# Performance work log

Measured on AMD Instinct MI355X. Metric: run time of the kernel, lower is better.

The kernel has to match this reference:

```python
import jax, jax.numpy as jnp
import numpy as np

EPS = 1e-12  # F.normalize eps

def _l2norm(x, axis=-1):
    n = jnp.linalg.norm(x, axis=axis, keepdims=True)
    return x / jnp.maximum(n, EPS)

def setup_inputs() -> dict:
    key = jax.random.key(0)
    k1, k2 = jax.random.split(key)
    Q, D = 512, 1024
    B, L = 64, 1024
    queries = jax.random.normal(k1, (Q, D), dtype=jnp.float32)
    local_tokens = jax.random.normal(k2, (B, L, D), dtype=jnp.float32)
    return {"queries": queries, "local_tokens": local_tokens}

def reference(queries, local_tokens):
    # sim_op == 'dot', repeat == True, need_attn_weights == False
    D = local_tokens.shape[-1]
    denom = jnp.sqrt(jnp.asarray(D, dtype=queries.dtype))
    # scores: [B, Q, L] == bmm(expand(queries), local_tokens^T) / sqrt(D)
    scores = jnp.einsum('qd,bld->bql', queries, local_tokens) / denom
    attn = jax.nn.softmax(scores, axis=-1)
    # aggregated: [B, Q, D]
    agg = jnp.einsum('bql,bld->bqd', attn, local_tokens)
    # post L2-normalize both sides (query normalize is batch-invariant)
    qn = _l2norm(queries)          # [Q, D]
    aggn = _l2norm(agg)            # [B, Q, D]
    # per-(b,q) dot product -> [B, Q], then transpose -> [Q, B]
    logits = jnp.einsum('qd,bqd->bq', qn, aggn).T
    return logits
```

## Files before the change

### kernel.cpp

```cpp
#include <hip/hip_runtime.h>
#include <stdint.h>

#define QN 512
#define DN 1024
#define BN 64
#define LN 1024

typedef _Float16 f16x8 __attribute__((ext_vector_type(8)));
typedef _Float16 f16x4 __attribute__((ext_vector_type(4)));
typedef float f32x4 __attribute__((ext_vector_type(4)));

#define DMA16(gp, lp)                                                        \
  __builtin_amdgcn_global_load_lds(                                          \
      (const __attribute__((address_space(1))) uint32_t*)(const void*)(gp),  \
      (__attribute__((address_space(3))) uint32_t*)(void*)(lp), 16, 0, 0)

__global__ __launch_bounds__(256) void k_convert(const float* __restrict__ tok,
                                                 _Float16* __restrict__ T,
                                                 _Float16* __restrict__ TT) {
  __shared__ __align__(16) _Float16 tile[64][68];
  const int b = blockIdx.z;
  const int l0 = blockIdx.y * 64, d0 = blockIdx.x * 64;
  const int tid = threadIdx.x;
  const int rr = tid >> 4;
  const int cq = tid & 15;
  const size_t base = (size_t)b * LN * DN;
#pragma unroll
  for (int p = 0; p < 4; ++p) {
    const int l = p * 16 + rr;
    const float4 v = *(const float4*)(tok + base + (size_t)(l0 + l) * DN + d0 + cq * 4);
    f16x4 hv;
    hv[0] = (_Float16)v.x; hv[1] = (_Float16)v.y; hv[2] = (_Float16)v.z; hv[3] = (_Float16)v.w;
    *(f16x4*)(T + base + (size_t)(l0 + l) * DN + d0 + cq * 4) = hv;
    tile[cq * 4 + 0][l] = hv[0];
    tile[cq * 4 + 1][l] = hv[1];
    tile[cq * 4 + 2][l] = hv[2];
    tile[cq * 4 + 3][l] = hv[3];
  }
  __syncthreads();
  const size_t baseT = (size_t)b * DN * LN;
#pragma unroll
  for (int p = 0; p < 4; ++p) {
    const int d = p * 16 + rr;
    const f16x4 hv = *(const f16x4*)(&tile[d][cq * 4]);
    *(f16x4*)(TT + baseT + (size_t)(d0 + d) * LN + l0 + cq * 4) = hv;
  }
}

__global__ __launch_bounds__(256) void k_queries(const float* __restrict__ q,
                                                 _Float16* __restrict__ Qh,
                                                 float* __restrict__ invqn) {
  const int qr = blockIdx.x;
  const int tid = threadIdx.x;
  const float4 v = *(const float4*)(q + (size_t)qr * DN + tid * 4);
  float ss = v.x * v.x + v.y * v.y + v.z * v.z + v.w * v.w;
#pragma unroll
  for (int off = 1; off < 64; off <<= 1) ss += __shfl_xor(ss, off, 64);
  __shared__ float red[4];
  if ((tid & 63) == 0) red[tid >> 6] = ss;
  __syncthreads();
  const float tot = red[0] + red[1] + red[2] + red[3];
  f16x4 hv;
  hv[0] = (_Float16)v.x; hv[1] = (_Float16)v.y; hv[2] = (_Float16)v.z; hv[3] = (_Float16)v.w;
  *(f16x4*)(Qh + (size_t)qr * DN + tid * 4) = hv;
  if (tid == 0) invqn[qr] = 1.0f / fmaxf(sqrtf(tot), 1e-12f);
}

__device__ __forceinline__ void decode_bq(int g, int& b, int& q0) {
  const int xcd = g & 7;
  const int t = g >> 3;
  const int qt8 = t & 7;
  b = ((t >> 3) << 3) | xcd;
  q0 = qt8 * 64;
}

__global__ __launch_bounds__(512, 2) void k_scores(const _Float16* __restrict__ Qh,
                                                   const _Float16* __restrict__ T,
                                                   _Float16* __restrict__ P,
                                                   float* __restrict__ numv) {
  __shared__ __align__(16) _Float16 Bb[2][32768];
  __shared__ float maxbuf[8][64];
  __shared__ float sumbuf[8][64];
  __shared__ float numbuf[8][64];
  __shared__ float Mbuf[64];
  __shared__ float Rbuf[64];
  int b, q0;
  decode_bq(blockIdx.x, b, q0);
  const int tid = threadIdx.x;
  const int w = tid >> 6, lane = tid & 63, c = lane & 15, quad = lane >> 4;

  const char* __restrict__ gT = (const char*)(T + (size_t)b * LN * DN);
  const _Float16* __restrict__ gA = Qh + (size_t)q0 * DN;

  const int r4 = lane >> 2;
  const int qsw = ((lane & 3) - ((lane >> 3) & 3)) & 3;
  const char* gBbase = gT + (size_t)(w * 128 + r4) * 2048 + qsw * 16;

  const int bswz = ((quad + ((c >> 1) & 3)) & 3) * 8;
  const int boff = (w * 128 + c) * 32 + bswz;

  f32x4 acc[4][8];
#pragma unroll
  for (int i = 0; i < 4; ++i)
#pragma unroll
    for (int j = 0; j < 8; ++j) acc[i][j] = 0.f;

  const _Float16* gAl = gA + (size_t)c * DN + quad * 8;

  f16x8 a_cur[4], a_nxt[4];
#pragma unroll
  for (int qt = 0; qt < 4; ++qt) a_cur[qt] = *(const f16x8*)(gAl + (size_t)qt * 16 * DN);
#pragma unroll
  for (int j = 0; j < 8; ++j) DMA16(gBbase + (size_t)j * 32768, &Bb[0][(w * 8 + j) * 512]);

  for (int s = 0; s < 31; ++s) {
    const int cur = s & 1;
    const int sn = s + 1;
#pragma unroll
    for (int qt = 0; qt < 4; ++qt)
      a_nxt[qt] = *(const f16x8*)(gAl + (size_t)qt * 16 * DN + sn * 32);
    asm volatile("s_waitcnt lgkmcnt(0)" ::: "memory");
#pragma unroll
    for (int j = 0; j < 8; ++j)
      DMA16(gBbase + (size_t)j * 32768 + sn * 64, &Bb[cur ^ 1][(w * 8 + j) * 512]);
    asm volatile("s_waitcnt vmcnt(12)" ::: "memory");
    __builtin_amdgcn_sched_barrier(0);

    const _Float16* __restrict__ Bp = &Bb[cur][0];
#pragma unroll
    for (int lt = 0; lt < 8; ++lt) {
      const f16x8 bv = *(const f16x8*)(Bp + boff + lt * 512);
#pragma unroll
      for (int qt = 0; qt < 4; ++qt)
        acc[qt][lt] = __builtin_amdgcn_mfma_f32_16x16x32_f16(a_cur[qt], bv, acc[qt][lt], 0, 0, 0);
    }
#pragma unroll
    for (int qt = 0; qt < 4; ++qt) a_cur[qt] = a_nxt[qt];
  }
  asm volatile("s_waitcnt vmcnt(0)" ::: "memory");
  __builtin_amdgcn_sched_barrier(0);
  {
    const _Float16* __restrict__ Bp = &Bb[1][0];
#pragma unroll
    for (int lt = 0; lt < 8; ++lt) {
      const f16x8 bv = *(const f16x8*)(Bp + boff + lt * 512);
#pragma unroll
      for (int qt = 0; qt < 4; ++qt)
        acc[qt][lt] = __builtin_amdgcn_mfma_f32_16x16x32_f16(a_cur[qt], bv, acc[qt][lt], 0, 0, 0);
    }
  }

  float mx[4][4];
#pragma unroll
  for (int qt = 0; qt < 4; ++qt)
#pragma unroll
    for (int r = 0; r < 4; ++r) {
      float m = acc[qt][0][r];
#pragma unroll
      for (int lt = 1; lt < 8; ++lt) m = fmaxf(m, acc[qt][lt][r]);
      mx[qt][r] = m;
    }
#pragma unroll
  for (int off = 1; off < 16; off <<= 1)
#pragma unroll
    for (int qt = 0; qt < 4; ++qt)
#pragma unroll
      for (int r = 0; r < 4; ++r) mx[qt][r] = fmaxf(mx[qt][r], __shfl_xor(mx[qt][r], off, 64));
  if (c == 0)
#pragma unroll
    for (int qt = 0; qt < 4; ++qt)
#pragma unroll
      for (int r = 0; r < 4; ++r) maxbuf[w][qt * 16 + quad * 4 + r] = mx[qt][r];
  __syncthreads();
  if (tid < 64) {
    float m = maxbuf[0][tid];
#pragma unroll
    for (int ww = 1; ww < 8; ++ww) m = fmaxf(m, maxbuf[ww][tid]);
    Mbuf[tid] = m;
  }
  __syncthreads();

  const float KE = 0.045084220027780106f;
  float Mr[4][4], sl[4][4], nl[4][4];
#pragma unroll
  for (int qt = 0; qt < 4; ++qt)
#pragma unroll
    for (int r = 0; r < 4; ++r) {
      Mr[qt][r] = Mbuf[qt * 16 + quad * 4 + r];
      sl[qt][r] = 0.f;
      nl[qt][r] = 0.f;
    }
#pragma unroll
  for (int qt = 0; qt < 4; ++qt)
#pragma unroll
    for (int lt = 0; lt < 8; ++lt)
#pragma unroll
      for (int r = 0; r < 4; ++r) {
        const float u = acc[qt][lt][r];
        const float p = exp2f((u - Mr[qt][r]) * KE);
        acc[qt][lt][r] = p;
        sl[qt][r] += p;
        nl[qt][r] += p * u;
      }
#pragma unroll
  for (int off = 1; off < 16; off <<= 1)
#pragma unroll
    for (int qt = 0; qt < 4; ++qt)
#pragma unroll
      for (int r = 0; r < 4; ++r) {
        sl[qt][r] += __shfl_xor(sl[qt][r], off, 64);
        nl[qt][r] += __shfl_xor(nl[qt][r], off, 64);
      }
  if (c == 0)
#pragma unroll
    for (int qt = 0; qt < 4; ++qt)
#pragma unroll
      for (int r = 0; r < 4; ++r) {
        sumbuf[w][qt * 16 + quad * 4 + r] = sl[qt][r];
        numbuf[w][qt * 16 + quad * 4 + r] = nl[qt][r];
      }
  __syncthreads();
  if (tid < 64) {
    float S = 0.f, N = 0.f;
#pragma unroll
    for (int ww = 0; ww < 8; ++ww) {
      S += sumbuf[ww][tid];
      N += numbuf[ww][tid];
    }
    Rbuf[tid] = 1.0f / S;
    numv[(size_t)b * QN + q0 + tid] = N / S;
  }
  __syncthreads();

  _Float16* Pb = P + ((size_t)b * QN + q0) * LN;
#pragma unroll
  for (int qt = 0; qt < 4; ++qt)
#pragma unroll
    for (int r = 0; r < 4; ++r) {
      const int row = qt * 16 + quad * 4 + r;
      const float rS = Rbuf[row];
      _Float16* prow = Pb + (size_t)row * LN + c;
#pragma unroll
      for (int lt = 0; lt < 8; ++lt) prow[w * 128 + lt * 16] = (_Float16)(acc[qt][lt][r] * rS);
    }
}

__global__ __launch_bounds__(512, 2) void k_agg(const _Float16* __restrict__ P,
                                                const _Float16* __restrict__ TT,
                                                float* __restrict__ norm2) {
  __shared__ __align__(16) _Float16 Bb[2][32768];
  __shared__ float redbuf[8][64];
  int b, q0;
  decode_bq(blockIdx.x, b, q0);
  const int tid = threadIdx.x;
  const int w = tid >> 6, lane = tid & 63, c = lane & 15, quad = lane >> 4;

  const char* __restrict__ gT = (const char*)(TT + (size_t)b * DN * LN);
  const _Float16* __restrict__ gA = P + ((size_t)b * QN + q0) * LN;

  const int r4 = lane >> 2;
  const int qsw = ((lane & 3) - ((lane >> 3) & 3)) & 3;
  const char* gBbase = gT + (size_t)(w * 128 + r4) * 2048 + qsw * 16;

  const int bswz = ((quad + ((c >> 1) & 3)) & 3) * 8;
  const int boff = (w * 128 + c) * 32 + bswz;

  f32x4 acc[4][8];
#pragma unroll
  for (int i = 0; i < 4; ++i)
#pragma unroll
    for (int j = 0; j < 8; ++j) acc[i][j] = 0.f;

  const _Float16* gAl = gA + (size_t)c * LN + quad * 8;

  f16x8 a_cur[4], a_nxt[4];
#pragma unroll
  for (int qt = 0; qt < 4; ++qt) a_cur[qt] = *(const f16x8*)(gAl + (size_t)qt * 16 * LN);
#pragma unroll
  for (int j = 0; j < 8; ++j) DMA16(gBbase + (size_t)j * 32768, &Bb[0][(w * 8 + j) * 512]);

  for (int s = 0; s < 31; ++s) {
    const int cur = s & 1;
    const int sn = s + 1;
#pragma unroll
    for (int qt = 0; qt < 4; ++qt)
      a_nxt[qt] = *(const f16x8*)(gAl + (size_t)qt * 16 * LN + sn * 32);
    asm volatile("s_waitcnt lgkmcnt(0)" ::: "memory");
#pragma unroll
    for (int j = 0; j < 8; ++j)
      DMA16(gBbase + (size_t)j * 32768 + sn * 64, &Bb[cur ^ 1][(w * 8 + j) * 512]);
    asm volatile("s_waitcnt vmcnt(12)" ::: "memory");
    __builtin_amdgcn_sched_barrier(0);

    const _Float16* __restrict__ Bp = &Bb[cur][0];
#pragma unroll
    for (int dt = 0; dt < 8; ++dt) {
      const f16x8 bv = *(const f16x8*)(Bp + boff + dt * 512);
#pragma unroll
      for (int qt = 0; qt < 4; ++qt)
        acc[qt][dt] = __builtin_amdgcn_mfma_f32_16x16x32_f16(a_cur[qt], bv, acc[qt][dt], 0, 0, 0);
    }
#pragma unroll
    for (int qt = 0; qt < 4; ++qt) a_cur[qt] = a_nxt[qt];
  }
  asm volatile("s_waitcnt vmcnt(0)" ::: "memory");
  __builtin_amdgcn_sched_barrier(0);
  {
    const _Float16* __restrict__ Bp = &Bb[1][0];
#pragma unroll
    for (int dt = 0; dt < 8; ++dt) {
      const f16x8 bv = *(const f16x8*)(Bp + boff + dt * 512);
#pragma unroll
      for (int qt = 0; qt < 4; ++qt)
        acc[qt][dt] = __builtin_amdgcn_mfma_f32_16x16x32_f16(a_cur[qt], bv, acc[qt][dt], 0, 0, 0);
    }
  }

  float ss[4][4];
#pragma unroll
  for (int qt = 0; qt < 4; ++qt)
#pragma unroll
    for (int r = 0; r < 4; ++r) {
      float s = 0.f;
#pragma unroll
      for (int dt = 0; dt < 8; ++dt) {
        const float v = acc[qt][dt][r];
        s += v * v;
      }
      ss[qt][r] = s;
    }
#pragma unroll
  for (int off = 1; off < 16; off <<= 1)
#pragma unroll
    for (int qt = 0; qt < 4; ++qt)
#pragma unroll
      for (int r = 0; r < 4; ++r) ss[qt][r] += __shfl_xor(ss[qt][r], off, 64);
  if (c == 0)
#pragma unroll
    for (int qt = 0; qt < 4; ++qt)
#pragma unroll
      for (int r = 0; r < 4; ++r) redbuf[w][qt * 16 + quad * 4 + r] = ss[qt][r];
  __syncthreads();
  if (tid < 64) {
    float s = 0.f;
#pragma unroll
    for (int ww = 0; ww < 8; ++ww) s += redbuf[ww][tid];
    norm2[(size_t)b * QN + q0 + tid] = s;
  }
}

__global__ __launch_bounds__(256) void k_final(const float* __restrict__ numv,
                                               const float* __restrict__ norm2,
                                               const float* __restrict__ invqn,
                                               float* __restrict__ out) {
  const int idx = blockIdx.x * 256 + threadIdx.x;
  const int q = idx >> 6, b = idx & 63;
  const float n = numv[(size_t)b * QN + q];
  const float d = sqrtf(norm2[(size_t)b * QN + q]);
  out[idx] = n * invqn[q] / fmaxf(d, 1e-12f);
}

extern "C" void kernel_launch(void* const* d_in, const int* in_sizes, int n_in,
                              void* d_out, int out_size, void* d_ws, size_t ws_size,
                              hipStream_t stream) {
  (void)in_sizes; (void)n_in; (void)out_size; (void)ws_size;
  const float* queries = (const float*)d_in[0];
  const float* tok = (const float*)d_in[1];
  float* out = (float*)d_out;
  char* ws = (char*)d_ws;

  _Float16* TT = (_Float16*)(ws + 0);
  _Float16* T = (_Float16*)(ws + 134217728);
  _Float16* P = (_Float16*)(ws + 268435456);
  _Float16* Qh = (_Float16*)(ws + 335544320);
  float* invqn = (float*)(ws + 336592896);
  float* numv = (float*)(ws + 336594944);
  float* norm2 = (float*)(ws + 336726016);

  hipLaunchKernelGGL(k_convert, dim3(16, 16, 64), dim3(256), 0, stream, tok, T, TT);
  hipLaunchKernelGGL(k_queries, dim3(512), dim3(256), 0, stream, queries, Qh, invqn);
  hipLaunchKernelGGL(k_scores, dim3(512), dim3(512), 0, stream, Qh, T, P, numv);
  hipLaunchKernelGGL(k_agg, dim3(512), dim3(512), 0, stream, P, TT, norm2);
  hipLaunchKernelGGL(k_final, dim3(128), dim3(256), 0, stream, numv, norm2, invqn, out);
}
```

Baseline: 680.7 us.

## Replace LDS double buffer with three-slot half-tile ring in scores and agg GEMMs

Both GEMM kernels now split each K-step's B tile into two half-tiles streamed through a three-slot LDS ring (48 KB instead of 64 KB), issuing the next DMA into a slot right after its fragments are read into registers. The MFMA blocks are wrapped in workgroup barriers with raised wave priority to keep the waves of a block in step. This aims to deepen prefetch and cut LDS footprint so that global-load latency is better hidden behind MFMA work. The extra s_barrier pairs per half-step add synchronisation cost, and the hand-tuned vmcnt counts have to match the DMA ordering exactly.

Result: slower. 711.2 us (+4.5%).

```diff
diff --git a/kernel.cpp b/kernel.cpp
--- a/kernel.cpp
+++ b/kernel.cpp
@@ -14,6 +14,19 @@
   __builtin_amdgcn_global_load_lds(                                          \
       (const __attribute__((address_space(1))) uint32_t*)(const void*)(gp),  \
       (__attribute__((address_space(3))) uint32_t*)(void*)(lp), 16, 0, 0)
+
+#define SBAR() __builtin_amdgcn_s_barrier()
+#define SCHED0() __builtin_amdgcn_sched_barrier(0)
+#define WAIT_VM(n)                                             \
+  do {                                                         \
+    asm volatile("s_waitcnt vmcnt(" #n ")" ::: "memory");      \
+    __builtin_amdgcn_sched_barrier(0);                         \
+  } while (0)
+#define WAIT_LGKM0()                                           \
+  do {                                                         \
+    asm volatile("s_waitcnt lgkmcnt(0)" ::: "memory");         \
+    __builtin_amdgcn_sched_barrier(0);                         \
+  } while (0)
 
 __global__ __launch_bounds__(256) void k_convert(const float* __restrict__ tok,
                                                  _Float16* __restrict__ T,
@@ -78,7 +91,7 @@
                                                    const _Float16* __restrict__ T,
                                                    _Float16* __restrict__ P,
                                                    float* __restrict__ numv) {
-  __shared__ __align__(16) _Float16 Bb[2][32768];
+  __shared__ __align__(16) _Float16 ring[3][16384];
   __shared__ float maxbuf[8][64];
   __shared__ float sumbuf[8][64];
   __shared__ float numbuf[8][64];
@@ -97,7 +110,8 @@
   const char* gBbase = gT + (size_t)(w * 128 + r4) * 2048 + qsw * 16;
 
   const int bswz = ((quad + ((c >> 1) & 3)) & 3) * 8;
-  const int boff = (w * 128 + c) * 32 + bswz;
+  const int fragoff = c * 32 + bswz;
+  const int slab0 = w * 4;
 
   f32x4 acc[4][8];
 #pragma unroll
@@ -109,45 +123,101 @@
 
   f16x8 a_cur[4], a_nxt[4];
 #pragma unroll
+  for (int jj = 0; jj < 4; ++jj)
+    DMA16(gBbase + (size_t)jj * 32768, &ring[0][(slab0 + jj) * 512]);
+  SCHED0();
+#pragma unroll
   for (int qt = 0; qt < 4; ++qt) a_cur[qt] = *(const f16x8*)(gAl + (size_t)qt * 16 * DN);
-#pragma unroll
-  for (int j = 0; j < 8; ++j) DMA16(gBbase + (size_t)j * 32768, &Bb[0][(w * 8 + j) * 512]);
-
+  SCHED0();
+#pragma unroll
+  for (int jj = 0; jj < 4; ++jj)
+    DMA16(gBbase + (size_t)(4 + jj) * 32768, &ring[1][(slab0 + jj) * 512]);
+#pragma unroll
+  for (int jj = 0; jj < 4; ++jj)
+    DMA16(gBbase + (size_t)jj * 32768 + 64, &ring[2][(slab0 + jj) * 512]);
+  SCHED0();
+
+  int rA = 0, rB = 1;
   for (int s = 0; s < 31; ++s) {
-    const int cur = s & 1;
-    const int sn = s + 1;
-#pragma unroll
-    for (int qt = 0; qt < 4; ++qt)
-      a_nxt[qt] = *(const f16x8*)(gAl + (size_t)qt * 16 * DN + sn * 32);
-    asm volatile("s_waitcnt lgkmcnt(0)" ::: "memory");
-#pragma unroll
-    for (int j = 0; j < 8; ++j)
-      DMA16(gBbase + (size_t)j * 32768 + sn * 64, &Bb[cur ^ 1][(w * 8 + j) * 512]);
-    asm volatile("s_waitcnt vmcnt(12)" ::: "memory");
-    __builtin_amdgcn_sched_barrier(0);
-
-    const _Float16* __restrict__ Bp = &Bb[cur][0];
-#pragma unroll
-    for (int lt = 0; lt < 8; ++lt) {
-      const f16x8 bv = *(const f16x8*)(Bp + boff + lt * 512);
+    WAIT_VM(12);
+    {
+      _Float16* rb = &ring[rA][0];
+      f16x8 bv[4];
+#pragma unroll
+      for (int jj = 0; jj < 4; ++jj) bv[jj] = *(const f16x8*)(rb + (slab0 + jj) * 512 + fragoff);
 #pragma unroll
       for (int qt = 0; qt < 4; ++qt)
-        acc[qt][lt] = __builtin_amdgcn_mfma_f32_16x16x32_f16(a_cur[qt], bv, acc[qt][lt], 0, 0, 0);
+        a_nxt[qt] = *(const f16x8*)(gAl + (size_t)qt * 16 * DN + (s + 1) * 32);
+      WAIT_LGKM0();
+#pragma unroll
+      for (int jj = 0; jj < 4; ++jj)
+        DMA16(gBbase + (size_t)(4 + jj) * 32768 + (s + 1) * 64, rb + (slab0 + jj) * 512);
+      SCHED0();
+      SBAR();
+      __builtin_amdgcn_s_setprio(1);
+#pragma unroll
+      for (int jj = 0; jj < 4; ++jj)
+#pragma unroll
+        for (int qt = 0; qt < 4; ++qt)
+          acc[qt][jj] = __builtin_amdgcn_mfma_f32_16x16x32_f16(a_cur[qt], bv[jj], acc[qt][jj], 0, 0, 0);
+      __builtin_amdgcn_s_setprio(0);
+      SBAR();
+    }
+    WAIT_VM(12);
+    {
+      _Float16* rb = &ring[rB][0];
+      f16x8 bv[4];
+#pragma unroll
+      for (int jj = 0; jj < 4; ++jj) bv[jj] = *(const f16x8*)(rb + (slab0 + jj) * 512 + fragoff);
+      WAIT_LGKM0();
+      if (s < 30) {
+#pragma unroll
+        for (int jj = 0; jj < 4; ++jj)
+          DMA16(gBbase + (size_t)jj * 32768 + (s + 2) * 64, rb + (slab0 + jj) * 512);
+      }
+      SCHED0();
+      SBAR();
+      __builtin_amdgcn_s_setprio(1);
+#pragma unroll
+      for (int jj = 0; jj < 4; ++jj)
+#pragma unroll
+        for (int qt = 0; qt < 4; ++qt)
+          acc[qt][4 + jj] =
+              __builtin_amdgcn_mfma_f32_16x16x32_f16(a_cur[qt], bv[jj], acc[qt][4 + jj], 0, 0, 0);
+      __builtin_amdgcn_s_setprio(0);
+      SBAR();
     }
 #pragma unroll
     for (int qt = 0; qt < 4; ++qt) a_cur[qt] = a_nxt[qt];
-  }
-  asm volatile("s_waitcnt vmcnt(0)" ::: "memory");
-  __builtin_amdgcn_sched_barrier(0);
+    rA += 2; if (rA >= 3) rA -= 3;
+    rB += 2; if (rB >= 3) rB -= 3;
+  }
+  WAIT_VM(8);
   {
-    const _Float16* __restrict__ Bp = &Bb[1][0];
-#pragma unroll
-    for (int lt = 0; lt < 8; ++lt) {
-      const f16x8 bv = *(const f16x8*)(Bp + boff + lt * 512);
+    _Float16* rb = &ring[rA][0];
+    f16x8 bv[4];
+#pragma unroll
+    for (int jj = 0; jj < 4; ++jj) bv[jj] = *(const f16x8*)(rb + (slab0 + jj) * 512 + fragoff);
+    WAIT_LGKM0();
+#pragma unroll
+    for (int jj = 0; jj < 4; ++jj)
 #pragma unroll
       for (int qt = 0; qt < 4; ++qt)
-        acc[qt][lt] = __builtin_amdgcn_mfma_f32_16x16x32_f16(a_cur[qt], bv, acc[qt][lt], 0, 0, 0);
-    }
+        acc[qt][jj] = __builtin_amdgcn_mfma_f32_16x16x32_f16(a_cur[qt], bv[jj], acc[qt][jj], 0, 0, 0);
+  }
+  WAIT_VM(0);
+  {
+    _Float16* rb = &ring[rB][0];
+    f16x8 bv[4];
+#pragma unroll
+    for (int jj = 0; jj < 4; ++jj) bv[jj] = *(const f16x8*)(rb + (slab0 + jj) * 512 + fragoff);
+    WAIT_LGKM0();
+#pragma unroll
+    for (int jj = 0; jj < 4; ++jj)
+#pragma unroll
+      for (int qt = 0; qt < 4; ++qt)
+        acc[qt][4 + jj] =
+            __builtin_amdgcn_mfma_f32_16x16x32_f16(a_cur[qt], bv[jj], acc[qt][4 + jj], 0, 0, 0);
   }
 
   float mx[4][4];
@@ -248,7 +318,7 @@
 __global__ __launch_bounds__(512, 2) void k_agg(const _Float16* __restrict__ P,
                                                 const _Float16* __restrict__ TT,
                                                 float* __restrict__ norm2) {
-  __shared__ __align__(16) _Float16 Bb[2][32768];
+  __shared__ __align__(16) _Float16 ring[3][16384];
   __shared__ float redbuf[8][64];
   int b, q0;
   decode_bq(blockIdx.x, b, q0);
@@ -263,7 +333,8 @@
   const char* gBbase = gT + (size_t)(w * 128 + r4) * 2048 + qsw * 16;
 
   const int bswz = ((quad + ((c >> 1) & 3)) & 3) * 8;
-  const int boff = (w * 128 + c) * 32 + bswz;
+  const int fragoff = c * 32 + bswz;
+  const int slab0 = w * 4;
 
   f32x4 acc[4][8];
 #pragma unroll
@@ -275,45 +346,101 @@
 
   f16x8 a_cur[4], a_nxt[4];
 #pragma unroll
+  for (int jj = 0; jj < 4; ++jj)
+    DMA16(gBbase + (size_t)jj * 32768, &ring[0][(slab0 + jj) * 512]);
+  SCHED0();
+#pragma unroll
   for (int qt = 0; qt < 4; ++qt) a_cur[qt] = *(const f16x8*)(gAl + (size_t)qt * 16 * LN);
-#pragma unroll
-  for (int j = 0; j < 8; ++j) DMA16(gBbase + (size_t)j * 32768, &Bb[0][(w * 8 + j) * 512]);
-
+  SCHED0();
+#pragma unroll
+  for (int jj = 0; jj < 4; ++jj)
+    DMA16(gBbase + (size_t)(4 + jj) * 32768, &ring[1][(slab0 + jj) * 512]);
+#pragma unroll
+  for (int jj = 0; jj < 4; ++jj)
+    DMA16(gBbase + (size_t)jj * 32768 + 64, &ring[2][(slab0 + jj) * 512]);
+  SCHED0();
+
+  int rA = 0, rB = 1;
   for (int s = 0; s < 31; ++s) {
-    const int cur = s & 1;
-    const int sn = s + 1;
-#pragma unroll
-    for (int qt = 0; qt < 4; ++qt)
-      a_nxt[qt] = *(const f16x8*)(gAl + (size_t)qt * 16 * LN + sn * 32);
-    asm volatile("s_waitcnt lgkmcnt(0)" ::: "memory");
-#pragma unroll
-    for (int j = 0; j < 8; ++j)
-      DMA16(gBbase + (size_t)j * 32768 + sn * 64, &Bb[cur ^ 1][(w * 8 + j) * 512]);
-    asm volatile("s_waitcnt vmcnt(12)" ::: "memory");
-    __builtin_amdgcn_sched_barrier(0);
-
-    const _Float16* __restrict__ Bp = &Bb[cur][0];
-#pragma unroll
-    for (int dt = 0; dt < 8; ++dt) {
-      const f16x8 bv = *(const f16x8*)(Bp + boff + dt * 512);
+    WAIT_VM(12);
+    {
+      _Float16* rb = &ring[rA][0];
+      f16x8 bv[4];
+#pragma unroll
+      for (int jj = 0; jj < 4; ++jj) bv[jj] = *(const f16x8*)(rb + (slab0 + jj) * 512 + fragoff);
 #pragma unroll
       for (int qt = 0; qt < 4; ++qt)
-        acc[qt][dt] = __builtin_amdgcn_mfma_f32_16x16x32_f16(a_cur[qt], bv, acc[qt][dt], 0, 0, 0);
+        a_nxt[qt] = *(const f16x8*)(gAl + (size_t)qt * 16 * LN + (s + 1) * 32);
+      WAIT_LGKM0();
+#pragma unroll
+      for (int jj = 0; jj < 4; ++jj)
+        DMA16(gBbase + (size_t)(4 + jj) * 32768 + (s + 1) * 64, rb + (slab0 + jj) * 512);
+      SCHED0();
+      SBAR();
+      __builtin_amdgcn_s_setprio(1);
+#pragma unroll
+      for (int jj = 0; jj < 4; ++jj)
+#pragma unroll
+        for (int qt = 0; qt < 4; ++qt)
+          acc[qt][jj] = __builtin_amdgcn_mfma_f32_16x16x32_f16(a_cur[qt], bv[jj], acc[qt][jj], 0, 0, 0);
+      __builtin_amdgcn_s_setprio(0);
+      SBAR();
+    }
+    WAIT_VM(12);
+    {
+      _Float16* rb = &ring[rB][0];
+      f16x8 bv[4];
+#pragma unroll
+      for (int jj = 0; jj < 4; ++jj) bv[jj] = *(const f16x8*)(rb + (slab0 + jj) * 512 + fragoff);
+      WAIT_LGKM0();
+      if (s < 30) {
+#pragma unroll
+        for (int jj = 0; jj < 4; ++jj)
+          DMA16(gBbase + (size_t)jj * 32768 + (s + 2) * 64, rb + (slab0 + jj) * 512);
+      }
+      SCHED0();
+      SBAR();
+      __builtin_amdgcn_s_setprio(1);
+#pragma unroll
+      for (int jj = 0; jj < 4; ++jj)
+#pragma unroll
+        for (int qt = 0; qt < 4; ++qt)
+          acc[qt][4 + jj] =
+              __builtin_amdgcn_mfma_f32_16x16x32_f16(a_cur[qt], bv[jj], acc[qt][4 + jj], 0, 0, 0);
+      __builtin_amdgcn_s_setprio(0);
+      SBAR();
     }
 #pragma unroll
     for (int qt = 0; qt < 4; ++qt) a_cur[qt] = a_nxt[qt];
-  }
-  asm volatile("s_waitcnt vmcnt(0)" ::: "memory");
-  __builtin_amdgcn_sched_barrier(0);
+    rA += 2; if (rA >= 3) rA -= 3;
+    rB += 2; if (rB >= 3) rB -= 3;
+  }
+  WAIT_VM(8);
   {
-    const _Float16* __restrict__ Bp = &Bb[1][0];
-#pragma unroll
-    for (int dt = 0; dt < 8; ++dt) {
-      const f16x8 bv = *(const f16x8*)(Bp + boff + dt * 512);
+    _Float16* rb = &ring[rA][0];
+    f16x8 bv[4];
+#pragma unroll
+    for (int jj = 0; jj < 4; ++jj) bv[jj] = *(const f16x8*)(rb + (slab0 + jj) * 512 + fragoff);
+    WAIT_LGKM0();
+#pragma unroll
+    for (int jj = 0; jj < 4; ++jj)
 #pragma unroll
       for (int qt = 0; qt < 4; ++qt)
-        acc[qt][dt] = __builtin_amdgcn_mfma_f32_16x16x32_f16(a_cur[qt], bv, acc[qt][dt], 0, 0, 0);
-    }
+        acc[qt][jj] = __builtin_amdgcn_mfma_f32_16x16x32_f16(a_cur[qt], bv[jj], acc[qt][jj], 0, 0, 0);
+  }
+  WAIT_VM(0);
+  {
+    _Float16* rb = &ring[rB][0];
+    f16x8 bv[4];
+#pragma unroll
+    for (int jj = 0; jj < 4; ++jj) bv[jj] = *(const f16x8*)(rb + (slab0 + jj) * 512 + fragoff);
+    WAIT_LGKM0();
+#pragma unroll
+    for (int jj = 0; jj < 4; ++jj)
+#pragma unroll
+      for (int qt = 0; qt < 4; ++qt)
+        acc[qt][4 + jj] =
+            __builtin_amdgcn_mfma_f32_16x16x32_f16(a_cur[qt], bv[jj], acc[qt][4 + jj], 0, 0, 0);
   }
 
   float ss[4][4];
```

## Pace sibling workgroups sharing a batch via global atomic counters for L2 reuse

Applied to the files above, without the earlier changes.

Adds per-(batch, wave, phase) atomic counters so the 8 workgroups that read the same batch's token tile line up every 8 k-steps, with a bounded spin of up to 320 polls. Keeping them in step is meant to make their shared B-tile reads hit in L2/MALL at the same time instead of drifting apart and re-fetching from HBM. In exchange it adds a full vmcnt(0) drain at each sync point, atomic traffic, spin-wait stalls, and an extra zeroing kernel launch.

Measured after the change: 826.4 us. 1.21x slower.

```diff
diff --git a/kernel.cpp b/kernel.cpp
--- a/kernel.cpp
+++ b/kernel.cpp
@@ -14,6 +14,11 @@
   __builtin_amdgcn_global_load_lds(                                          \
       (const __attribute__((address_space(1))) uint32_t*)(const void*)(gp),  \
       (__attribute__((address_space(3))) uint32_t*)(void*)(lp), 16, 0, 0)
+
+__global__ __launch_bounds__(256) void k_zero(int* __restrict__ cnt) {
+  const int i = blockIdx.x * 256 + threadIdx.x;
+  if (i < 4096) cnt[i] = 0;
+}
 
 __global__ __launch_bounds__(256) void k_convert(const float* __restrict__ tok,
                                                  _Float16* __restrict__ T,
@@ -74,10 +79,21 @@
   q0 = qt8 * 64;
 }
 
+__device__ __forceinline__ void pace_couple(int* __restrict__ cnt, int b, int w, int s,
+                                            int lane) {
+  int* cp = cnt + (b * 8 + w) * 4 + (s >> 3);
+  if (lane == 0) __hip_atomic_fetch_add(cp, 1, __ATOMIC_RELAXED, __HIP_MEMORY_SCOPE_AGENT);
+  for (int p = 0; p < 320; ++p) {
+    if (__hip_atomic_load(cp, __ATOMIC_RELAXED, __HIP_MEMORY_SCOPE_AGENT) >= 8) break;
+    asm volatile("" ::: "memory");
+  }
+}
+
 __global__ __launch_bounds__(512, 2) void k_scores(const _Float16* __restrict__ Qh,
                                                    const _Float16* __restrict__ T,
                                                    _Float16* __restrict__ P,
-                                                   float* __restrict__ numv) {
+                                                   float* __restrict__ numv,
+                                                   int* __restrict__ cnt) {
   __shared__ __align__(16) _Float16 Bb[2][32768];
   __shared__ float maxbuf[8][64];
   __shared__ float sumbuf[8][64];
@@ -114,6 +130,12 @@
   for (int j = 0; j < 8; ++j) DMA16(gBbase + (size_t)j * 32768, &Bb[0][(w * 8 + j) * 512]);
 
   for (int s = 0; s < 31; ++s) {
+    if ((s & 7) == 0 && s != 0) {
+      asm volatile("s_waitcnt vmcnt(0)" ::: "memory");
+      __builtin_amdgcn_sched_barrier(0);
+      pace_couple(cnt, b, w, s, lane);
+      __builtin_amdgcn_sched_barrier(0);
+    }
     const int cur = s & 1;
     const int sn = s + 1;
 #pragma unroll
@@ -247,7 +269,8 @@
 
 __global__ __launch_bounds__(512, 2) void k_agg(const _Float16* __restrict__ P,
                                                 const _Float16* __restrict__ TT,
-                                                float* __restrict__ norm2) {
+                                                float* __restrict__ norm2,
+                                                int* __restrict__ cnt) {
   __shared__ __align__(16) _Float16 Bb[2][32768];
   __shared__ float redbuf[8][64];
   int b, q0;
@@ -280,6 +303,12 @@
   for (int j = 0; j < 8; ++j) DMA16(gBbase + (size_t)j * 32768, &Bb[0][(w * 8 + j) * 512]);
 
   for (int s = 0; s < 31; ++s) {
+    if ((s & 7) == 0 && s != 0) {
+      asm volatile("s_waitcnt vmcnt(0)" ::: "memory");
+      __builtin_amdgcn_sched_barrier(0);
+      pace_couple(cnt, b, w, s, lane);
+      __builtin_amdgcn_sched_barrier(0);
+    }
     const int cur = s & 1;
     const int sn = s + 1;
 #pragma unroll
@@ -376,10 +405,12 @@
   float* invqn = (float*)(ws + 336592896);
   float* numv = (float*)(ws + 336594944);
   float* norm2 = (float*)(ws + 336726016);
-
+  int* cnt = (int*)(ws + 336857088);
+
+  hipLaunchKernelGGL(k_zero, dim3(16), dim3(256), 0, stream, cnt);
   hipLaunchKernelGGL(k_convert, dim3(16, 16, 64), dim3(256), 0, stream, tok, T, TT);
   hipLaunchKernelGGL(k_queries, dim3(512), dim3(256), 0, stream, queries, Qh, invqn);
-  hipLaunchKernelGGL(k_scores, dim3(512), dim3(512), 0, stream, Qh, T, P, numv);
-  hipLaunchKernelGGL(k_agg, dim3(512), dim3(512), 0, stream, P, TT, norm2);
+  hipLaunchKernelGGL(k_scores, dim3(512), dim3(512), 0, stream, Qh, T, P, numv, cnt);
+  hipLaunchKernelGGL(k_agg, dim3(512), dim3(512), 0, stream, P, TT, norm2, cnt + 2048);
   hipLaunchKernelGGL(k_final, dim3(128), dim3(256), 0, stream, numv, norm2, invqn, out);
 }
```

## Pre-tile fp16 token buffers into swizzled LDS-ready slabs for contiguous DMA

Applied to the files above, without the earlier changes.

The convert kernel now writes both the fp16 token copy and its transpose in a blocked layout. Each 32-wide k-step slab is stored exactly as the swizzled LDS image the GEMM kernels expect. The scores and aggregation kernels can then issue fully contiguous 1 KB-per-wave global-to-LDS DMA loads instead of strided 64-byte row fragments. The goal is better global memory coalescing and less address arithmetic in the main loops, at the cost of scattered 8-byte stores in the conversion kernel.

Result: faster. 650.1 us (-4.5%).

```diff
diff --git a/kernel.cpp b/kernel.cpp
--- a/kernel.cpp
+++ b/kernel.cpp
@@ -16,34 +16,47 @@
       (__attribute__((address_space(3))) uint32_t*)(void*)(lp), 16, 0, 0)
 
 __global__ __launch_bounds__(256) void k_convert(const float* __restrict__ tok,
-                                                 _Float16* __restrict__ T,
-                                                 _Float16* __restrict__ TT) {
+                                                 _Float16* __restrict__ T2,
+                                                 _Float16* __restrict__ TT2) {
   __shared__ __align__(16) _Float16 tile[64][68];
   const int b = blockIdx.z;
   const int l0 = blockIdx.y * 64, d0 = blockIdx.x * 64;
   const int tid = threadIdx.x;
   const int rr = tid >> 4;
   const int cq = tid & 15;
+  const int g = (cq >> 1) & 3;
+  const int e0 = (cq & 1) * 4;
+  const int sq = cq >> 3;
   const size_t base = (size_t)b * LN * DN;
+  const size_t ib = (size_t)b * 1048576;
 #pragma unroll
   for (int p = 0; p < 4; ++p) {
-    const int l = p * 16 + rr;
-    const float4 v = *(const float4*)(tok + base + (size_t)(l0 + l) * DN + d0 + cq * 4);
+    const int l = l0 + p * 16 + rr;
+    const float4 v = *(const float4*)(tok + base + (size_t)l * DN + d0 + cq * 4);
     f16x4 hv;
     hv[0] = (_Float16)v.x; hv[1] = (_Float16)v.y; hv[2] = (_Float16)v.z; hv[3] = (_Float16)v.w;
-    *(f16x4*)(T + base + (size_t)(l0 + l) * DN + d0 + cq * 4) = hv;
-    tile[cq * 4 + 0][l] = hv[0];
-    tile[cq * 4 + 1][l] = hv[1];
-    tile[cq * 4 + 2][l] = hv[2];
-    tile[cq * 4 + 3][l] = hv[3];
-  }
-  __syncthreads();
-  const size_t baseT = (size_t)b * DN * LN;
+    const int s = (d0 >> 5) + sq;
+    const int slab = l >> 4, r4 = l & 15;
+    const int m = (g + ((r4 >> 1) & 3)) & 3;
+    const int off = slab * 512 + (r4 * 4 + m) * 8 + e0;
+    *(f16x4*)(T2 + ib + (size_t)s * 32768 + off) = hv;
+    const int ll = p * 16 + rr;
+    tile[cq * 4 + 0][ll] = hv[0];
+    tile[cq * 4 + 1][ll] = hv[1];
+    tile[cq * 4 + 2][ll] = hv[2];
+    tile[cq * 4 + 3][ll] = hv[3];
+  }
+  __syncthreads();
 #pragma unroll
   for (int p = 0; p < 4; ++p) {
-    const int d = p * 16 + rr;
-    const f16x4 hv = *(const f16x4*)(&tile[d][cq * 4]);
-    *(f16x4*)(TT + baseT + (size_t)(d0 + d) * LN + l0 + cq * 4) = hv;
+    const int dl = p * 16 + rr;
+    const int d = d0 + dl;
+    const f16x4 hv = *(const f16x4*)(&tile[dl][cq * 4]);
+    const int s2 = (l0 >> 5) + sq;
+    const int slab = d >> 4, r4 = d & 15;
+    const int m = (g + ((r4 >> 1) & 3)) & 3;
+    const int off = slab * 512 + (r4 * 4 + m) * 8 + e0;
+    *(f16x4*)(TT2 + ib + (size_t)s2 * 32768 + off) = hv;
   }
 }
 
@@ -75,7 +88,7 @@
 }
 
 __global__ __launch_bounds__(512, 2) void k_scores(const _Float16* __restrict__ Qh,
-                                                   const _Float16* __restrict__ T,
+                                                   const _Float16* __restrict__ T2,
                                                    _Float16* __restrict__ P,
                                                    float* __restrict__ numv) {
   __shared__ __align__(16) _Float16 Bb[2][32768];
@@ -89,12 +102,8 @@
   const int tid = threadIdx.x;
   const int w = tid >> 6, lane = tid & 63, c = lane & 15, quad = lane >> 4;
 
-  const char* __restrict__ gT = (const char*)(T + (size_t)b * LN * DN);
+  const char* __restrict__ gB = (const char*)(T2 + (size_t)b * 1048576) + lane * 16;
   const _Float16* __restrict__ gA = Qh + (size_t)q0 * DN;
-
-  const int r4 = lane >> 2;
-  const int qsw = ((lane & 3) - ((lane >> 3) & 3)) & 3;
-  const char* gBbase = gT + (size_t)(w * 128 + r4) * 2048 + qsw * 16;
 
   const int bswz = ((quad + ((c >> 1) & 3)) & 3) * 8;
   const int boff = (w * 128 + c) * 32 + bswz;
@@ -111,7 +120,8 @@
 #pragma unroll
   for (int qt = 0; qt < 4; ++qt) a_cur[qt] = *(const f16x8*)(gAl + (size_t)qt * 16 * DN);
 #pragma unroll
-  for (int j = 0; j < 8; ++j) DMA16(gBbase + (size_t)j * 32768, &Bb[0][(w * 8 + j) * 512]);
+  for (int j = 0; j < 8; ++j)
+    DMA16(gB + (size_t)(w * 8 + j) * 1024, &Bb[0][(w * 8 + j) * 512]);
 
   for (int s = 0; s < 31; ++s) {
     const int cur = s & 1;
@@ -122,7 +132,7 @@
     asm volatile("s_waitcnt lgkmcnt(0)" ::: "memory");
 #pragma unroll
     for (int j = 0; j < 8; ++j)
-      DMA16(gBbase + (size_t)j * 32768 + sn * 64, &Bb[cur ^ 1][(w * 8 + j) * 512]);
+      DMA16(gB + (size_t)sn * 65536 + (size_t)(w * 8 + j) * 1024, &Bb[cur ^ 1][(w * 8 + j) * 512]);
     asm volatile("s_waitcnt vmcnt(12)" ::: "memory");
     __builtin_amdgcn_sched_barrier(0);
 
@@ -246,7 +256,7 @@
 }
 
 __global__ __launch_bounds__(512, 2) void k_agg(const _Float16* __restrict__ P,
-                                                const _Float16* __restrict__ TT,
+                                                const _Float16* __restrict__ TT2,
                                                 float* __restrict__ norm2) {
   __shared__ __align__(16) _Float16 Bb[2][32768];
   __shared__ float redbuf[8][64];
@@ -255,12 +265,8 @@
   const int tid = threadIdx.x;
   const int w = tid >> 6, lane = tid & 63, c = lane & 15, quad = lane >> 4;
 
-  const char* __restrict__ gT = (const char*)(TT + (size_t)b * DN * LN);
+  const char* __restrict__ gB = (const char*)(TT2 + (size_t)b * 1048576) + lane * 16;
   const _Float16* __restrict__ gA = P + ((size_t)b * QN + q0) * LN;
-
-  const int r4 = lane >> 2;
-  const int qsw = ((lane & 3) - ((lane >> 3) & 3)) & 3;
-  const char* gBbase = gT + (size_t)(w * 128 + r4) * 2048 + qsw * 16;
 
   const int bswz = ((quad + ((c >> 1) & 3)) & 3) * 8;
   const int boff = (w * 128 + c) * 32 + bswz;
@@ -277,7 +283,8 @@
 #pragma unroll
   for (int qt = 0; qt < 4; ++qt) a_cur[qt] = *(const f16x8*)(gAl + (size_t)qt * 16 * LN);
 #pragma unroll
-  for (int j = 0; j < 8; ++j) DMA16(gBbase + (size_t)j * 32768, &Bb[0][(w * 8 + j) * 512]);
+  for (int j = 0; j < 8; ++j)
+    DMA16(gB + (size_t)(w * 8 + j) * 1024, &Bb[0][(w * 8 + j) * 512]);
 
   for (int s = 0; s < 31; ++s) {
     const int cur = s & 1;
@@ -288,7 +295,7 @@
     asm volatile("s_waitcnt lgkmcnt(0)" ::: "memory");
 #pragma unroll
     for (int j = 0; j < 8; ++j)
-      DMA16(gBbase + (size_t)j * 32768 + sn * 64, &Bb[cur ^ 1][(w * 8 + j) * 512]);
+      DMA16(gB + (size_t)sn * 65536 + (size_t)(w * 8 + j) * 1024, &Bb[cur ^ 1][(w * 8 + j) * 512]);
     asm volatile("s_waitcnt vmcnt(12)" ::: "memory");
     __builtin_amdgcn_sched_barrier(0);
 
@@ -369,17 +376,17 @@
   float* out = (float*)d_out;
   char* ws = (char*)d_ws;
 
-  _Float16* TT = (_Float16*)(ws + 0);
-  _Float16* T = (_Float16*)(ws + 134217728);
+  _Float16* T2 = (_Float16*)(ws + 0);
+  _Float16* TT2 = (_Float16*)(ws + 134217728);
   _Float16* P = (_Float16*)(ws + 268435456);
   _Float16* Qh = (_Float16*)(ws + 335544320);
   float* invqn = (float*)(ws + 336592896);
   float* numv = (float*)(ws + 336594944);
   float* norm2 = (float*)(ws + 336726016);
 
-  hipLaunchKernelGGL(k_convert, dim3(16, 16, 64), dim3(256), 0, stream, tok, T, TT);
+  hipLaunchKernelGGL(k_convert, dim3(16, 16, 64), dim3(256), 0, stream, tok, T2, TT2);
   hipLaunchKernelGGL(k_queries, dim3(512), dim3(256), 0, stream, queries, Qh, invqn);
-  hipLaunchKernelGGL(k_scores, dim3(512), dim3(512), 0, stream, Qh, T, P, numv);
-  hipLaunchKernelGGL(k_agg, dim3(512), dim3(512), 0, stream, P, TT, norm2);
+  hipLaunchKernelGGL(k_scores, dim3(512), dim3(512), 0, stream, Qh, T2, P, numv);
+  hipLaunchKernelGGL(k_agg, dim3(512), dim3(512), 0, stream, P, TT2, norm2);
   hipLaunchKernelGGL(k_final, dim3(128), dim3(256), 0, stream, numv, norm2, invqn, out);
 }
```
